# Optimization experiments

Hardware: AMD Instinct MI355X
Metric: run time of the kernel (lower is better)

Reference implementation:

```python
import jax, jax.numpy as jnp
import numpy as np

N = 50000    # nodes
E = 800000   # edges (avg degree 16)
IN, H, OUT = 128, 16, 300


def setup_inputs() -> dict:
    key = jax.random.key(0)
    ks = jax.random.split(key, 8)
    x = jax.random.normal(ks[0], (N, IN), jnp.float32)
    edge_index = jax.random.randint(ks[1], (2, E), 0, N, jnp.int32)

    def w(k, i, o):
        return jax.random.normal(k, (i, o), jnp.float32) / np.float32(np.sqrt(i))

    return dict(
        x=x, edge_index=edge_index,
        W1=w(ks[2], IN, H), b1=jnp.zeros((H,), jnp.float32),
        Wl1=w(ks[3], IN, H), bl1=jnp.zeros((H,), jnp.float32),
        W2=w(ks[4], H, H), b2=jnp.zeros((H,), jnp.float32),
        Wl2=w(ks[5], H, H), bl2=jnp.zeros((H,), jnp.float32),
        Wo=w(ks[6], H, OUT), bo=jnp.zeros((OUT,), jnp.float32),
    )


def gcn_conv(x, W, b, src, dst, n):
    """PyG GCNConv: x@W, symmetric norm with self-loops, scatter-add, + bias."""
    h = x @ W                                    # [N, F_out]
    ones = jnp.ones(src.shape[0], h.dtype)
    deg = jax.ops.segment_sum(ones, dst, num_segments=n) + 1.0  # +1 self-loop
    dinv = jax.lax.rsqrt(deg)                    # deg >= 1, safe
    norm = dinv[src] * dinv[dst]                 # [E]
    agg = jax.ops.segment_sum(h[src] * norm[:, None], dst, num_segments=n)
    agg = agg + h * (dinv * dinv)[:, None]       # self-loop message
    return agg + b


def reference(x, edge_index, W1, b1, Wl1, bl1, W2, b2, Wl2, bl2, Wo, bo):
    src, dst = edge_index[0], edge_index[1]
    n = x.shape[0]
    # layer 1: conv.relu + skip linear  (dropout p=0 / inference -> identity)
    h = jax.nn.relu(gcn_conv(x, W1, b1, src, dst, n)) + (x @ Wl1 + bl1)
    # layer 2
    h = jax.nn.relu(gcn_conv(h, W2, b2, src, dst, n)) + (h @ Wl2 + bl2)
    # output conv + log_softmax over classes
    out = gcn_conv(h, Wo, bo, src, dst, n)
    return jax.nn.log_softmax(out, axis=1)
```

## Files before the change

### kernel.cpp

```cpp
#include <hip/hip_runtime.h>
#include <hip/hip_bf16.h>

#define NN   50000
#define EE   800000
#define INF_ 128
#define HH   16
#define OUTC 300

#define NB   196
#define CAP  4608
#define CHK  4096
#define GB_  196

#define W1_OFF   0
#define WL1_OFF  2048
#define B1_OFF   4096
#define BL1_OFF  4112
#define W2_OFF   4128
#define WL2_OFF  4384
#define B2_OFF   4640
#define BL2_OFF  4656
#define WO_OFF   4672
#define BO_OFF   9472
#define WC_TOT   9772

__device__ __forceinline__ float bfu2f(unsigned short u) {
    return __uint_as_float(((unsigned)u) << 16);
}
__device__ __forceinline__ unsigned short f2bfu(float f) {
    __hip_bfloat16 h = __float2bfloat16(f);
    return *reinterpret_cast<unsigned short*>(&h);
}
__device__ __forceinline__ unsigned packbf(float lo, float hi) {
    return (unsigned)f2bfu(lo) | ((unsigned)f2bfu(hi) << 16);
}
__device__ __forceinline__ float cvt1(const void* p, int i, int flag) {
    return flag ? ((const float*)p)[i] : bfu2f(((const unsigned short*)p)[i]);
}
__device__ __forceinline__ float louf(unsigned u) { return __uint_as_float(u << 16); }
__device__ __forceinline__ float hiuf(unsigned u) { return __uint_as_float(u & 0xffff0000u); }

__global__ __launch_bounds__(256) void convert_kernel(
    const void* __restrict__ W1, const void* __restrict__ Wl1,
    const void* __restrict__ b1, const void* __restrict__ bl1,
    const void* __restrict__ W2, const void* __restrict__ Wl2,
    const void* __restrict__ b2, const void* __restrict__ bl2,
    const void* __restrict__ Wo, const void* __restrict__ bo,
    const unsigned* __restrict__ xw, int* __restrict__ flagp,
    int* __restrict__ gcur, float* __restrict__ wc)
{
    __shared__ int shits;
    int tid = threadIdx.x;
    if (tid == 0) shits = 0;
    __syncthreads();
    unsigned w = xw[tid];
    float lo = __uint_as_float(w << 16);
    if (!(fabsf(lo) < 1e4f)) atomicAdd(&shits, 1);
    __syncthreads();
    const int flag = (shits > 8) ? 1 : 0;

    if (blockIdx.x == 0) {
        if (tid == 0) flagp[0] = flag;
        if (tid < NB) gcur[tid] = 0;
    }

    int t = blockIdx.x * 256 + tid;
    if (t >= WC_TOT) return;
    float v;
    if      (t < WL1_OFF) v = cvt1(W1,  t - W1_OFF,  flag);
    else if (t < B1_OFF)  v = cvt1(Wl1, t - WL1_OFF, flag);
    else if (t < BL1_OFF) v = cvt1(b1,  t - B1_OFF,  flag);
    else if (t < W2_OFF)  v = cvt1(bl1, t - BL1_OFF, flag);
    else if (t < WL2_OFF) v = cvt1(W2,  t - W2_OFF,  flag);
    else if (t < B2_OFF)  v = cvt1(Wl2, t - WL2_OFF, flag);
    else if (t < BL2_OFF) v = cvt1(b2,  t - B2_OFF,  flag);
    else if (t < WO_OFF)  v = cvt1(bl2, t - BL2_OFF, flag);
    else if (t < BO_OFF)  v = cvt1(Wo,  t - WO_OFF,  flag);
    else                  v = cvt1(bo,  t - BO_OFF,  flag);
    wc[t] = v;
}

__global__ __launch_bounds__(256) void bplace_kernel(
    const int* __restrict__ src, const int* __restrict__ dst,
    int* __restrict__ gcur, uint2* __restrict__ gpairs)
{
    __shared__ uint2 raw[CHK];
    __shared__ uint2 srt[CHK];
    __shared__ unsigned char bid[CHK];
    __shared__ int cnt[NB];
    __shared__ int loff[NB];
    __shared__ int cur2[NB];
    __shared__ int gbase[NB];
    __shared__ int sc[256];

    int tid = threadIdx.x;
    int e0 = blockIdx.x * CHK;
    int n = min(CHK, EE - e0);
    if (n <= 0) return;
    for (int t = tid; t < NB; t += 256) cnt[t] = 0;
    __syncthreads();

    for (int j = tid; j < n; j += 256) {
        unsigned s = (unsigned)src[e0 + j];
        unsigned d = (unsigned)dst[e0 + j];
        raw[j] = make_uint2(s, d);
        atomicAdd(&cnt[d >> 8], 1);
    }
    __syncthreads();

    int v = (tid < NB) ? cnt[tid] : 0;
    sc[tid] = v;
    __syncthreads();
    for (int d = 1; d < 256; d <<= 1) {
        int u = (tid >= d) ? sc[tid - d] : 0;
        __syncthreads();
        sc[tid] += u;
        __syncthreads();
    }
    if (tid < NB) { loff[tid] = sc[tid] - v; cur2[tid] = sc[tid] - v; }
    __syncthreads();

    for (int j = tid; j < n; j += 256) {
        uint2 p = raw[j];
        int b = (int)(p.y >> 8);
        int pos = atomicAdd(&cur2[b], 1);
        srt[pos] = p;
        bid[pos] = (unsigned char)b;
    }
    __syncthreads();

    if (tid < NB) {
        int c = cnt[tid];
        gbase[tid] = c ? atomicAdd(&gcur[tid], c) : 0;
    }
    __syncthreads();

    for (int j = tid; j < n; j += 256) {
        int b = bid[j];
        int p = gbase[b] + (j - loff[b]);
        if (p < CAP) gpairs[(size_t)b * CAP + p] = srt[j];
    }
}

__global__ __launch_bounds__(256) void cplace_kernel(
    const uint2* __restrict__ gpairs, const int* __restrict__ gcur,
    int* __restrict__ off, float* __restrict__ dinv, int* __restrict__ csr_src)
{
    __shared__ uint2 pl[CAP];
    __shared__ int sc[256];
    __shared__ int ncnt[256];
    __shared__ int nscan[256];
    __shared__ int ncur[256];
    int b = blockIdx.x, t = threadIdx.x;

    int bv = (t < NB) ? gcur[t] : 0;
    sc[t] = bv;
    __syncthreads();
    for (int d = 1; d < 256; d <<= 1) {
        int u = (t >= d) ? sc[t - d] : 0;
        __syncthreads();
        sc[t] += u;
        __syncthreads();
    }
    __shared__ int gb_s;
    if (t == b) gb_s = sc[t] - bv;
    if (b == 0 && t == 0) off[NN] = EE;
    ncnt[t] = 0;
    __syncthreads();
    int gb = gb_s;

    int c = min(gcur[b], CAP);
    int nb = b << 8;
    for (int j = t; j < c; j += 256) pl[j] = gpairs[(size_t)b * CAP + j];
    __syncthreads();

    for (int j = t; j < c; j += 256) atomicAdd(&ncnt[pl[j].y & 255], 1);
    __syncthreads();

    int v = ncnt[t];
    nscan[t] = v;
    __syncthreads();
    for (int d = 1; d < 256; d <<= 1) {
        int u = (t >= d) ? nscan[t - d] : 0;
        __syncthreads();
        nscan[t] += u;
        __syncthreads();
    }
    int excl = nscan[t] - v;
    ncur[t] = excl;

    int node = nb + t;
    if (node < NN) {
        off[node] = gb + excl;
        dinv[node] = rsqrtf((float)v + 1.0f);
    }
    __syncthreads();

    for (int j = t; j < c; j += 256) {
        uint2 p = pl[j];
        int d = (int)(p.y & 255);
        int pos = atomicAdd(&ncur[d], 1);
        csr_src[gb + pos] = (int)p.x;
    }
}

__global__ __launch_bounds__(256) void lin1_kernel(
    const void* __restrict__ xp, const float* __restrict__ wc,
    const float* __restrict__ dinv, const int* __restrict__ flagp,
    unsigned short* __restrict__ A, unsigned short* __restrict__ B)
{
    __shared__ float2 sWL[INF_ * HH];
    __shared__ float sb[HH];
    for (int t = threadIdx.x; t < INF_ * HH; t += 256)
        sWL[t] = make_float2(wc[W1_OFF + t], wc[WL1_OFF + t]);
    if (threadIdx.x < HH) sb[threadIdx.x] = wc[BL1_OFF + threadIdx.x];
    __syncthreads();

    int i = blockIdx.x * 256 + threadIdx.x;
    if (i >= NN) return;
    const int flag = flagp[0];

    float a[HH], l[HH];
#pragma unroll
    for (int f = 0; f < HH; f++) { a[f] = 0.f; l[f] = 0.f; }

    for (int k0 = 0; k0 < INF_ / 8; k0++) {
        float xv[8];
        if (flag) {
            const float4* xr = (const float4*)((const float*)xp + (size_t)i * INF_);
            float4 r0 = xr[k0 * 2], r1 = xr[k0 * 2 + 1];
            xv[0] = r0.x; xv[1] = r0.y; xv[2] = r0.z; xv[3] = r0.w;
            xv[4] = r1.x; xv[5] = r1.y; xv[6] = r1.z; xv[7] = r1.w;
        } else {
            const uint4* xr = (const uint4*)((const unsigned short*)xp + (size_t)i * INF_);
            uint4 v = xr[k0];
            unsigned uu[4] = { v.x, v.y, v.z, v.w };
#pragma unroll
            for (int q = 0; q < 4; q++) {
                xv[q * 2]     = __uint_as_float(uu[q] << 16);
                xv[q * 2 + 1] = __uint_as_float(uu[q] & 0xffff0000u);
            }
        }
#pragma unroll
        for (int j = 0; j < 8; j++) {
            float xj = xv[j];
            int k = k0 * 8 + j;
#pragma unroll
            for (int f = 0; f < HH; f++) {
                float2 wv = sWL[k * HH + f];
                a[f] = fmaf(xj, wv.x, a[f]);
                l[f] = fmaf(xj, wv.y, l[f]);
            }
        }
    }
    float di = dinv[i];
    unsigned pa[8], pb[8];
#pragma unroll
    for (int h = 0; h < 8; h++) {
        pa[h] = packbf(a[2 * h] * di, a[2 * h + 1] * di);
        pb[h] = packbf(l[2 * h] + sb[2 * h], l[2 * h + 1] + sb[2 * h + 1]);
    }
    uint4* Ar = (uint4*)(A + (size_t)i * HH);
    uint4* Br = (uint4*)(B + (size_t)i * HH);
    Ar[0] = make_uint4(pa[0], pa[1], pa[2], pa[3]);
    Ar[1] = make_uint4(pa[4], pa[5], pa[6], pa[7]);
    Br[0] = make_uint4(pb[0], pb[1], pb[2], pb[3]);
    Br[1] = make_uint4(pb[4], pb[5], pb[6], pb[7]);
}

__global__ __launch_bounds__(256) void gather_combine_kernel(
    const int* __restrict__ off, const int* __restrict__ csr,
    const float* __restrict__ dinv, const unsigned short* __restrict__ X,
    unsigned short* __restrict__ Y, const float* __restrict__ bias, int mode)
{
    int lane = threadIdx.x & 63;
    int w = (blockIdx.x * 256 + threadIdx.x) >> 6;
    int n = lane >> 4, j = lane & 15;
    int node = w * 4 + n;
    int s0 = off[node], s1 = off[node + 1];
    int deg = s1 - s0;

    int wmax = deg;
    wmax = max(wmax, __shfl_xor(wmax, 16));
    wmax = max(wmax, __shfl_xor(wmax, 32));

    const uint2* X4 = (const uint2*)X;
    float a0 = 0.f, a1 = 0.f, a2 = 0.f, a3 = 0.f;
    int eh = j >> 2, q = j & 3;

    for (int base = 0; base < wmax; base += 16) {
        int p = s0 + base + j;
        int sj = (p < s1) ? csr[p] : 0;
#pragma unroll
        for (int r = 0; r < 4; r++) {
            int e = r * 4 + eh;
            int se = __shfl(sj, (n << 4) + e);
            bool val = (base + e) < deg;
            uint2 v = X4[(size_t)(val ? se : node) * 4 + q];
            if (val) {
                a0 += louf(v.x); a1 += hiuf(v.x);
                a2 += louf(v.y); a3 += hiuf(v.y);
            }
        }
    }
#pragma unroll
    for (int m = 4; m <= 8; m <<= 1) {
        a0 += __shfl_xor(a0, m);
        a1 += __shfl_xor(a1, m);
        a2 += __shfl_xor(a2, m);
        a3 += __shfl_xor(a3, m);
    }
    if (eh == 0) {
        float di = dinv[node];
        uint2 xv = X4[(size_t)node * 4 + q];
        float x0 = louf(xv.x), x1 = hiuf(xv.x), x2 = louf(xv.y), x3 = hiuf(xv.y);
        float o0, o1, o2, o3;
        if (mode == 2) {
            o0 = di * (a0 + x0); o1 = di * (a1 + x1);
            o2 = di * (a2 + x2); o3 = di * (a3 + x3);
        } else {
            uint2 yv = ((const uint2*)Y)[(size_t)node * 4 + q];
            float y0 = louf(yv.x), y1 = hiuf(yv.x), y2 = louf(yv.y), y3 = hiuf(yv.y);
            o0 = fmaxf(di * (a0 + x0) + bias[q * 4 + 0], 0.f) + y0;
            o1 = fmaxf(di * (a1 + x1) + bias[q * 4 + 1], 0.f) + y1;
            o2 = fmaxf(di * (a2 + x2) + bias[q * 4 + 2], 0.f) + y2;
            o3 = fmaxf(di * (a3 + x3) + bias[q * 4 + 3], 0.f) + y3;
            if (mode) { o0 *= di; o1 *= di; o2 *= di; o3 *= di; }
        }
        ((uint2*)Y)[(size_t)node * 4 + q] = make_uint2(packbf(o0, o1), packbf(o2, o3));
    }
}

__global__ __launch_bounds__(256) void gather_lin2_kernel(
    const int* __restrict__ off, const int* __restrict__ csr,
    const float* __restrict__ dinv, const unsigned short* __restrict__ X,
    const unsigned short* __restrict__ Yin, const float* __restrict__ wc,
    unsigned short* __restrict__ A2, unsigned short* __restrict__ B2)
{
    int lane = threadIdx.x & 63;
    int w = (blockIdx.x * 256 + threadIdx.x) >> 6;
    int n = lane >> 4, j = lane & 15;
    int node = w * 4 + n;
    int s0 = off[node], s1 = off[node + 1];
    int deg = s1 - s0;

    int wmax = deg;
    wmax = max(wmax, __shfl_xor(wmax, 16));
    wmax = max(wmax, __shfl_xor(wmax, 32));

    const uint2* X4 = (const uint2*)X;
    float a0 = 0.f, a1 = 0.f, a2 = 0.f, a3 = 0.f;
    int eh = j >> 2, q = j & 3;

    for (int base = 0; base < wmax; base += 16) {
        int p = s0 + base + j;
        int sj = (p < s1) ? csr[p] : 0;
#pragma unroll
        for (int r = 0; r < 4; r++) {
            int e = r * 4 + eh;
            int se = __shfl(sj, (n << 4) + e);
            bool val = (base + e) < deg;
            uint2 v = X4[(size_t)(val ? se : node) * 4 + q];
            if (val) {
                a0 += louf(v.x); a1 += hiuf(v.x);
                a2 += louf(v.y); a3 += hiuf(v.y);
            }
        }
    }
#pragma unroll
    for (int m = 4; m <= 8; m <<= 1) {
        a0 += __shfl_xor(a0, m);
        a1 += __shfl_xor(a1, m);
        a2 += __shfl_xor(a2, m);
        a3 += __shfl_xor(a3, m);
    }
    float di = dinv[node];
    uint2 xv = X4[(size_t)node * 4 + q];
    uint2 yv = ((const uint2*)Yin)[(size_t)node * 4 + q];
    float4 bq = ((const float4*)(wc + B1_OFF))[q];
    float o0 = fmaxf(di * (a0 + louf(xv.x)) + bq.x, 0.f) + louf(yv.x);
    float o1 = fmaxf(di * (a1 + hiuf(xv.x)) + bq.y, 0.f) + hiuf(yv.x);
    float o2 = fmaxf(di * (a2 + louf(xv.y)) + bq.z, 0.f) + louf(yv.y);
    float o3 = fmaxf(di * (a3 + hiuf(xv.y)) + bq.w, 0.f) + hiuf(yv.y);

    int f = j;
    float a = 0.f, l = 0.f;
#pragma unroll
    for (int k = 0; k < HH; k++) {
        int srcl = (lane & 48) + (k >> 2);
        float hk;
        if      ((k & 3) == 0) hk = __shfl(o0, srcl);
        else if ((k & 3) == 1) hk = __shfl(o1, srcl);
        else if ((k & 3) == 2) hk = __shfl(o2, srcl);
        else                   hk = __shfl(o3, srcl);
        a = fmaf(hk, wc[W2_OFF  + k * HH + f], a);
        l = fmaf(hk, wc[WL2_OFF + k * HH + f], l);
    }
    A2[(size_t)node * HH + f] = f2bfu(a * di);
    B2[(size_t)node * HH + f] = f2bfu(l + wc[BL2_OFF + f]);
}

__global__ __launch_bounds__(256) void final_kernel(
    const unsigned short* __restrict__ Z, const float* __restrict__ wc,
    const int* __restrict__ flagp, void* __restrict__ outp)
{
    const float* Wo = wc + WO_OFF;
    const float* bo = wc + BO_OFF;
    const int flag = flagp[0];
    int wave = threadIdx.x >> 6, lane = threadIdx.x & 63;
    int i0 = blockIdx.x * 16 + wave * 4;

    float zf[4];
#pragma unroll
    for (int n = 0; n < 4; n++) zf[n] = bfu2f(Z[(size_t)(i0 + n) * HH + (lane & 15)]);

    const bool tl = (lane < OUTC - 256);
    float4 bq = *(const float4*)(bo + lane * 4);
    float bt = tl ? bo[256 + lane] : 0.f;

    float y[4][4], yt[4];
#pragma unroll
    for (int n = 0; n < 4; n++) {
        y[n][0] = bq.x; y[n][1] = bq.y; y[n][2] = bq.z; y[n][3] = bq.w;
        yt[n] = bt;
    }

#pragma unroll
    for (int k = 0; k < HH; k++) {
        const float* wr = Wo + k * OUTC;
        float4 wq = *(const float4*)(wr + lane * 4);
        float wt = tl ? wr[256 + lane] : 0.f;
        float zb[4];
#pragma unroll
        for (int n = 0; n < 4; n++) zb[n] = __shfl(zf[n], k);
#pragma unroll
        for (int n = 0; n < 4; n++) {
            y[n][0] = fmaf(zb[n], wq.x, y[n][0]);
            y[n][1] = fmaf(zb[n], wq.y, y[n][1]);
            y[n][2] = fmaf(zb[n], wq.z, y[n][2]);
            y[n][3] = fmaf(zb[n], wq.w, y[n][3]);
            yt[n]   = fmaf(zb[n], wt,   yt[n]);
        }
    }

#pragma unroll
    for (int n = 0; n < 4; n++) {
        float m = fmaxf(fmaxf(y[n][0], y[n][1]), fmaxf(y[n][2], y[n][3]));
        if (tl) m = fmaxf(m, yt[n]);
#pragma unroll
        for (int o = 32; o > 0; o >>= 1) m = fmaxf(m, __shfl_xor(m, o));
        float s = __expf(y[n][0] - m) + __expf(y[n][1] - m)
                + __expf(y[n][2] - m) + __expf(y[n][3] - m);
        if (tl) s += __expf(yt[n] - m);
#pragma unroll
        for (int o = 32; o > 0; o >>= 1) s += __shfl_xor(s, o);
        float lse = m + __logf(s);

        if (flag) {
            float* orow = (float*)outp + (size_t)(i0 + n) * OUTC;
            *(float4*)(orow + lane * 4) = make_float4(
                y[n][0] - lse, y[n][1] - lse, y[n][2] - lse, y[n][3] - lse);
            if (tl) orow[256 + lane] = yt[n] - lse;
        } else {
            unsigned short* orow = (unsigned short*)outp + (size_t)(i0 + n) * OUTC;
            *(uint2*)(orow + lane * 4) = make_uint2(
                packbf(y[n][0] - lse, y[n][1] - lse),
                packbf(y[n][2] - lse, y[n][3] - lse));
            if (tl) orow[256 + lane] = f2bfu(yt[n] - lse);
        }
    }
}

extern "C" void kernel_launch(void* const* d_in, const int* in_sizes, int n_in,
                              void* d_out, int out_size, void* d_ws, size_t ws_size,
                              hipStream_t stream) {
    const void* x   = d_in[0];
    const int*  ei  = (const int*)d_in[1];
    const void* W1  = d_in[2];
    const void* b1  = d_in[3];
    const void* Wl1 = d_in[4];
    const void* bl1 = d_in[5];
    const void* W2  = d_in[6];
    const void* b2  = d_in[7];
    const void* Wl2 = d_in[8];
    const void* bl2 = d_in[9];
    const void* Wo  = d_in[10];
    const void* bo  = d_in[11];

    const int* srcp = ei;
    const int* dstp = ei + EE;

    char* wsb = (char*)d_ws;
    int*   flag    = (int*)wsb;
    float* wc      = (float*)(wsb + 4 * 16);
    int*   gcur    = (int*)(wsb + 4 * 10000);
    int*   off     = (int*)(wsb + 4 * 10400);
    int*   csr_src = (int*)(wsb + 4 * 60416);
    float* dinv    = (float*)(wsb + 4 * 860416);
    uint2* gpairs  = (uint2*)(wsb + 4 * 910416);
    unsigned short* A  = (unsigned short*)(wsb + 4 * 2716752);
    unsigned short* B  = (unsigned short*)(wsb + 4 * 3116752);
    unsigned short* A2 = (unsigned short*)(wsb + 4 * 3516752);
    unsigned short* B2 = (unsigned short*)(wsb + 4 * 3916752);

    const int gN  = (NN + 255) / 256;
    const int gG4 = (NN / 4 * 64) / 256;
    const int gW  = (WC_TOT + 255) / 256;

    convert_kernel<<<gW, 256, 0, stream>>>(W1, Wl1, b1, bl1, W2, Wl2, b2, bl2,
                                           Wo, bo, (const unsigned*)x, flag, gcur, wc);

    bplace_kernel<<<GB_, 256, 0, stream>>>(srcp, dstp, gcur, gpairs);
    cplace_kernel<<<NB, 256, 0, stream>>>(gpairs, gcur, off, dinv, csr_src);

    lin1_kernel<<<gN, 256, 0, stream>>>(x, wc, dinv, flag, A, B);
    gather_lin2_kernel<<<gG4, 256, 0, stream>>>(off, csr_src, dinv, A, B, wc, A2, B2);

    gather_combine_kernel<<<gG4, 256, 0, stream>>>(off, csr_src, dinv, A2, B2, wc + B2_OFF, 1);

    gather_combine_kernel<<<gG4, 256, 0, stream>>>(off, csr_src, dinv, B2, A, wc + B2_OFF, 2);

    final_kernel<<<gG4, 256, 0, stream>>>(A, wc, flag, d_out);
}
```

Before: 215.6 us.

## Replace two-level bucket CSR build with global-atomic count, scan, and place

The CSR construction changes from a two-pass bucketed approach, which sorted edges into 196 coarse buckets in shared memory and then placed them per node, to a simpler scheme. Per-node degrees are counted with global atomics inside the weight-convert kernel, a two-kernel prefix scan follows, and a place kernel scatters sources using a global atomic cursor per node. This drops large shared-memory staging and the intermediate pair buffer, but adds 800K contended global atomics twice, more launches, and nondeterministic edge order within each row.

```diff
diff --git a/kernel.cpp b/kernel.cpp
--- a/kernel.cpp
+++ b/kernel.cpp
@@ -8,9 +8,7 @@
 #define OUTC 300
 
 #define NB   196
-#define CAP  4608
-#define CHK  4096
-#define GB_  196
+#define GE_  3125
 
 #define W1_OFF   0
 #define WL1_OFF  2048
@@ -40,14 +38,20 @@
 __device__ __forceinline__ float louf(unsigned u) { return __uint_as_float(u << 16); }
 __device__ __forceinline__ float hiuf(unsigned u) { return __uint_as_float(u & 0xffff0000u); }
 
-__global__ __launch_bounds__(256) void convert_kernel(
+__global__ __launch_bounds__(256) void zero_kernel(int* __restrict__ deg)
+{
+    int node = blockIdx.x * 256 + threadIdx.x;
+    if (node < NN) deg[node] = 0;
+}
+
+__global__ __launch_bounds__(256) void convert_count_kernel(
     const void* __restrict__ W1, const void* __restrict__ Wl1,
     const void* __restrict__ b1, const void* __restrict__ bl1,
     const void* __restrict__ W2, const void* __restrict__ Wl2,
     const void* __restrict__ b2, const void* __restrict__ bl2,
     const void* __restrict__ Wo, const void* __restrict__ bo,
-    const unsigned* __restrict__ xw, int* __restrict__ flagp,
-    int* __restrict__ gcur, float* __restrict__ wc)
+    const unsigned* __restrict__ xw, const int* __restrict__ dst,
+    int* __restrict__ flagp, int* __restrict__ deg, float* __restrict__ wc)
 {
     __shared__ int shits;
     int tid = threadIdx.x;
@@ -59,13 +63,13 @@
     __syncthreads();
     const int flag = (shits > 8) ? 1 : 0;
 
-    if (blockIdx.x == 0) {
-        if (tid == 0) flagp[0] = flag;
-        if (tid < NB) gcur[tid] = 0;
-    }
-
-    int t = blockIdx.x * 256 + tid;
-    if (t >= WC_TOT) return;
+    if (blockIdx.x == 0 && tid == 0) flagp[0] = flag;
+
+    int gid = blockIdx.x * 256 + tid;
+    atomicAdd(&deg[dst[gid]], 1);
+
+    if (gid >= WC_TOT) return;
+    int t = gid;
     float v;
     if      (t < WL1_OFF) v = cvt1(W1,  t - W1_OFF,  flag);
     else if (t < B1_OFF)  v = cvt1(Wl1, t - WL1_OFF, flag);
@@ -80,81 +84,15 @@
     wc[t] = v;
 }
 
-__global__ __launch_bounds__(256) void bplace_kernel(
-    const int* __restrict__ src, const int* __restrict__ dst,
-    int* __restrict__ gcur, uint2* __restrict__ gpairs)
-{
-    __shared__ uint2 raw[CHK];
-    __shared__ uint2 srt[CHK];
-    __shared__ unsigned char bid[CHK];
-    __shared__ int cnt[NB];
-    __shared__ int loff[NB];
-    __shared__ int cur2[NB];
-    __shared__ int gbase[NB];
+__global__ __launch_bounds__(256) void scan1_kernel(
+    const int* __restrict__ deg, int* __restrict__ off,
+    float* __restrict__ dinv, int* __restrict__ bsum)
+{
     __shared__ int sc[256];
-
-    int tid = threadIdx.x;
-    int e0 = blockIdx.x * CHK;
-    int n = min(CHK, EE - e0);
-    if (n <= 0) return;
-    for (int t = tid; t < NB; t += 256) cnt[t] = 0;
-    __syncthreads();
-
-    for (int j = tid; j < n; j += 256) {
-        unsigned s = (unsigned)src[e0 + j];
-        unsigned d = (unsigned)dst[e0 + j];
-        raw[j] = make_uint2(s, d);
-        atomicAdd(&cnt[d >> 8], 1);
-    }
-    __syncthreads();
-
-    int v = (tid < NB) ? cnt[tid] : 0;
-    sc[tid] = v;
-    __syncthreads();
-    for (int d = 1; d < 256; d <<= 1) {
-        int u = (tid >= d) ? sc[tid - d] : 0;
-        __syncthreads();
-        sc[tid] += u;
-        __syncthreads();
-    }
-    if (tid < NB) { loff[tid] = sc[tid] - v; cur2[tid] = sc[tid] - v; }
-    __syncthreads();
-
-    for (int j = tid; j < n; j += 256) {
-        uint2 p = raw[j];
-        int b = (int)(p.y >> 8);
-        int pos = atomicAdd(&cur2[b], 1);
-        srt[pos] = p;
-        bid[pos] = (unsigned char)b;
-    }
-    __syncthreads();
-
-    if (tid < NB) {
-        int c = cnt[tid];
-        gbase[tid] = c ? atomicAdd(&gcur[tid], c) : 0;
-    }
-    __syncthreads();
-
-    for (int j = tid; j < n; j += 256) {
-        int b = bid[j];
-        int p = gbase[b] + (j - loff[b]);
-        if (p < CAP) gpairs[(size_t)b * CAP + p] = srt[j];
-    }
-}
-
-__global__ __launch_bounds__(256) void cplace_kernel(
-    const uint2* __restrict__ gpairs, const int* __restrict__ gcur,
-    int* __restrict__ off, float* __restrict__ dinv, int* __restrict__ csr_src)
-{
-    __shared__ uint2 pl[CAP];
-    __shared__ int sc[256];
-    __shared__ int ncnt[256];
-    __shared__ int nscan[256];
-    __shared__ int ncur[256];
     int b = blockIdx.x, t = threadIdx.x;
-
-    int bv = (t < NB) ? gcur[t] : 0;
-    sc[t] = bv;
+    int node = b * 256 + t;
+    int v = (node < NN) ? deg[node] : 0;
+    sc[t] = v;
     __syncthreads();
     for (int d = 1; d < 256; d <<= 1) {
         int u = (t >= d) ? sc[t - d] : 0;
@@ -162,46 +100,49 @@
         sc[t] += u;
         __syncthreads();
     }
+    if (node < NN) {
+        off[node] = sc[t] - v;
+        dinv[node] = rsqrtf((float)v + 1.0f);
+    }
+    if (t == 255) bsum[b] = sc[255];
+}
+
+__global__ __launch_bounds__(256) void scan2_kernel(
+    const int* __restrict__ bsum, int* __restrict__ off, int* __restrict__ cur)
+{
+    __shared__ int sc[256];
     __shared__ int gb_s;
+    int b = blockIdx.x, t = threadIdx.x;
+    int bv = (t < NB) ? bsum[t] : 0;
+    sc[t] = bv;
+    __syncthreads();
+    for (int d = 1; d < 256; d <<= 1) {
+        int u = (t >= d) ? sc[t - d] : 0;
+        __syncthreads();
+        sc[t] += u;
+        __syncthreads();
+    }
     if (t == b) gb_s = sc[t] - bv;
+    __syncthreads();
+    int gb = gb_s;
+
+    int node = b * 256 + t;
+    if (node < NN) {
+        int o = off[node] + gb;
+        off[node] = o;
+        cur[node] = o;
+    }
     if (b == 0 && t == 0) off[NN] = EE;
-    ncnt[t] = 0;
-    __syncthreads();
-    int gb = gb_s;
-
-    int c = min(gcur[b], CAP);
-    int nb = b << 8;
-    for (int j = t; j < c; j += 256) pl[j] = gpairs[(size_t)b * CAP + j];
-    __syncthreads();
-
-    for (int j = t; j < c; j += 256) atomicAdd(&ncnt[pl[j].y & 255], 1);
-    __syncthreads();
-
-    int v = ncnt[t];
-    nscan[t] = v;
-    __syncthreads();
-    for (int d = 1; d < 256; d <<= 1) {
-        int u = (t >= d) ? nscan[t - d] : 0;
-        __syncthreads();
-        nscan[t] += u;
-        __syncthreads();
-    }
-    int excl = nscan[t] - v;
-    ncur[t] = excl;
-
-    int node = nb + t;
-    if (node < NN) {
-        off[node] = gb + excl;
-        dinv[node] = rsqrtf((float)v + 1.0f);
-    }
-    __syncthreads();
-
-    for (int j = t; j < c; j += 256) {
-        uint2 p = pl[j];
-        int d = (int)(p.y & 255);
-        int pos = atomicAdd(&ncur[d], 1);
-        csr_src[gb + pos] = (int)p.x;
-    }
+}
+
+__global__ __launch_bounds__(256) void place_kernel(
+    const int* __restrict__ src, const int* __restrict__ dst,
+    int* __restrict__ cur, int* __restrict__ csr)
+{
+    int gid = blockIdx.x * 256 + threadIdx.x;
+    int s = src[gid], d = dst[gid];
+    int pos = atomicAdd(&cur[d], 1);
+    csr[pos] = s;
 }
 
 __global__ __launch_bounds__(256) void lin1_kernel(
@@ -493,25 +434,28 @@
     char* wsb = (char*)d_ws;
     int*   flag    = (int*)wsb;
     float* wc      = (float*)(wsb + 4 * 16);
-    int*   gcur    = (int*)(wsb + 4 * 10000);
-    int*   off     = (int*)(wsb + 4 * 10400);
-    int*   csr_src = (int*)(wsb + 4 * 60416);
-    float* dinv    = (float*)(wsb + 4 * 860416);
-    uint2* gpairs  = (uint2*)(wsb + 4 * 910416);
-    unsigned short* A  = (unsigned short*)(wsb + 4 * 2716752);
-    unsigned short* B  = (unsigned short*)(wsb + 4 * 3116752);
-    unsigned short* A2 = (unsigned short*)(wsb + 4 * 3516752);
-    unsigned short* B2 = (unsigned short*)(wsb + 4 * 3916752);
+    int*   deg     = (int*)(wsb + 4 * 12288);
+    int*   bsum    = (int*)(wsb + 4 * 62400);
+    int*   off     = (int*)(wsb + 4 * 62608);
+    int*   cur     = (int*)(wsb + 4 * 112624);
+    float* dinv    = (float*)(wsb + 4 * 162640);
+    int*   csr_src = (int*)(wsb + 4 * 212656);
+    unsigned short* A  = (unsigned short*)(wsb + 4 * 1012672);
+    unsigned short* B  = (unsigned short*)(wsb + 4 * 1412672);
+    unsigned short* A2 = (unsigned short*)(wsb + 4 * 1812672);
+    unsigned short* B2 = (unsigned short*)(wsb + 4 * 2212672);
 
     const int gN  = (NN + 255) / 256;
     const int gG4 = (NN / 4 * 64) / 256;
-    const int gW  = (WC_TOT + 255) / 256;
-
-    convert_kernel<<<gW, 256, 0, stream>>>(W1, Wl1, b1, bl1, W2, Wl2, b2, bl2,
-                                           Wo, bo, (const unsigned*)x, flag, gcur, wc);
-
-    bplace_kernel<<<GB_, 256, 0, stream>>>(srcp, dstp, gcur, gpairs);
-    cplace_kernel<<<NB, 256, 0, stream>>>(gpairs, gcur, off, dinv, csr_src);
+
+    zero_kernel<<<NB, 256, 0, stream>>>(deg);
+    convert_count_kernel<<<GE_, 256, 0, stream>>>(W1, Wl1, b1, bl1, W2, Wl2,
+                                                  b2, bl2, Wo, bo,
+                                                  (const unsigned*)x, dstp,
+                                                  flag, deg, wc);
+    scan1_kernel<<<NB, 256, 0, stream>>>(deg, off, dinv, bsum);
+    scan2_kernel<<<NB, 256, 0, stream>>>(bsum, off, cur);
+    place_kernel<<<GE_, 256, 0, stream>>>(srcp, dstp, cur, csr_src);
 
     lin1_kernel<<<gN, 256, 0, stream>>>(x, wc, dinv, flag, A, B);
     gather_lin2_kernel<<<gG4, 256, 0, stream>>>(off, csr_src, dinv, A, B, wc, A2, B2);
```

After: 279.1 us. 1.29x slower.
